# Optimization experiments

Hardware: AMD Instinct MI355X
Metric: run time of the kernel (lower is better)

Reference implementation:

```python
import jax, jax.numpy as jnp
import numpy as np

PI = 3.14159265359
FC = 5.208e6; FS = 20.832e6; FDEMOD = 5.208e6; C = 1540.0
FNUM = 2.0; MINW = 1e-3
NANG = 4; NELEM = 128; NZ = 192; NX = 192; NSAMP = 2048


def setup_inputs() -> dict:
    key = jax.random.key(0)
    k1, k2 = jax.random.split(key)
    idata = jax.random.normal(k1, (NANG, NELEM, NSAMP), jnp.float32)
    qdata = jax.random.normal(k2, (NANG, NELEM, NSAMP), jnp.float32)
    pitch = 0.298e-3  # PICMUS L11 pitch [m]
    ex = (np.arange(NELEM) - (NELEM - 1) / 2.0) * pitch
    ele_pos = np.stack([ex, np.zeros(NELEM), np.zeros(NELEM)], -1).astype(np.float32)
    xs = np.linspace(ex[0], ex[-1], NX)
    zs = np.linspace(5e-3, 48e-3, NZ)
    zz, xx = np.meshgrid(zs, xs, indexing='ij')  # out_shape = (NZ, NX)
    grid = np.stack([xx.ravel(), np.zeros(NZ * NX), zz.ravel()], -1).astype(np.float32)
    angles = np.linspace(-0.16, 0.16, NANG).astype(np.float32)
    time_zero = np.zeros(NANG, np.float32)
    return {"idata": idata, "qdata": qdata, "grid": jnp.asarray(grid),
            "angles": jnp.asarray(angles), "ele_pos": jnp.asarray(ele_pos),
            "time_zero": jnp.asarray(time_zero)}


def _lerp_gather(data, i0, frac):
    # data: [A,E,S]; i0: [A,E,P] int32; zero-padding outside [0,S) (grid_sample zeros, align_corners=False)
    S = data.shape[-1]
    def samp(idx):
        valid = (idx >= 0) & (idx < S)
        g = jnp.take_along_axis(data, jnp.clip(idx, 0, S - 1), axis=-1)
        return jnp.where(valid, g, jnp.zeros((), data.dtype))
    return (1.0 - frac) * samp(i0) + frac * samp(i0 + 1)


def reference(idata, qdata, grid, angles, ele_pos, time_zero):
    x = grid[:, 0]; z = grid[:, 2]  # [P]
    sin_a = jnp.sin(angles); cos_a = jnp.cos(angles)
    # -- transmit delays (plane wave) and apodization --  [A,P]
    txdel = (x[None, :] * sin_a[:, None] + z[None, :] * cos_a[:, None]
             + time_zero[:, None] * C) * (FS / C)
    xlim0 = ele_pos[0, 0]; xlim1 = ele_pos[-1, 0]
    x_proj = x[None, :] - z[None, :] * jnp.tan(angles)[:, None]
    txapo = ((x_proj >= xlim0 * 1.2) & (x_proj <= xlim1 * 1.2)).astype(idata.dtype)
    # -- receive delays (focus) and dynamic-aperture apodization --  [E,P]
    v = grid[None, :, :] - ele_pos[:, None, :]  # [E,P,3]
    rxdel = jnp.sqrt(jnp.sum(v * v, axis=-1)) * (FS / C)
    vx = v[..., 0]; vz = v[..., 2]
    mask = jnp.abs(vz / vx) > FNUM
    mask = mask | (jnp.abs(vx) <= MINW)
    mask = mask | ((vx >= MINW) & (x[None, :] <= ele_pos[0, 0]))
    mask = mask | ((vx <= -MINW) & (x[None, :] >= ele_pos[-1, 0]))
    rxapo = mask.astype(idata.dtype)
    # -- total delays and linear interpolation of IQ (grid_sample bilinear, H=1) --
    delays = txdel[:, None, :] + rxdel[None, :, :]  # [A,E,P] in samples
    i0f = jnp.floor(delays)
    frac = delays - i0f
    i0 = i0f.astype(jnp.int32)
    ifoc = _lerp_gather(idata, i0, frac)
    qfoc = _lerp_gather(qdata, i0, frac)
    # -- demodulation phase rotation --
    tshift = delays / FS - z[None, None, :] * 2.0 / C
    theta = 2.0 * PI * FDEMOD * tshift
    ct = jnp.cos(theta); st = jnp.sin(theta)
    ir = ifoc * ct - qfoc * st
    qr = qfoc * ct + ifoc * st
    # -- apodize and accumulate over angles and elements --
    apod = txapo[:, None, :] * rxapo[None, :, :]
    idas = jnp.sum(ir * apod, axis=(0, 1)).reshape(NZ, NX)
    qdas = jnp.sum(qr * apod, axis=(0, 1)).reshape(NZ, NX)
    return (idas, qdas)
```

## Files before the change

kernel.cpp:

```cpp
#include <hip/hip_runtime.h>
#include <math.h>

#define NANG   4
#define NELEM  128
#define NSAMP  2048
#define NZ     192
#define NX     192
#define NPIX   (NZ * NX)
#define NCHUNK 8
#define ECHUNK (NELEM / NCHUNK)
#define XT     16
#define ZT     4
#define NXT    (NX / XT)
#define NZT    (NZ / ZT)

constexpr float C_SOUND = 1540.0f;
constexpr float FS      = 20832000.0f;
constexpr float FDEMOD  = 5208000.0f;
constexpr float FS_C    = FS / C_SOUND;

__global__ __launch_bounds__(256) void das_pw_kernel(
    const float* __restrict__ idata,
    const float* __restrict__ qdata,
    const float* __restrict__ grid,
    const float* __restrict__ angles,
    const float* __restrict__ ele_pos,
    const float* __restrict__ time_zero,
    float* __restrict__ out)
{
    const int lane = threadIdx.x;
    const int a    = threadIdx.y;

    const int x0c = ((int)blockIdx.x % NXT) * XT;
    const int z0r = ((int)blockIdx.x / NXT) * ZT;

    const float ex0    = ele_pos[0];
    const float inv_pe = 1.0f / (ele_pos[3] - ex0);
    const float xlimN  = ele_pos[3 * (NELEM - 1)];
    const float xmin   = grid[3 * (z0r * NX + x0c)];
    const float xmax   = grid[3 * (z0r * NX + x0c + XT - 1)];
    const float zmax   = grid[3 * ((z0r + ZT - 1) * NX + x0c) + 2];
    const float half   = 0.5f * zmax;

    int e_lo = (int)floorf((xmin - half - ex0) * inv_pe);
    int e_hi = (int)ceilf ((xmax + half - ex0) * inv_pe) + 1;
    const int c0 = (int)blockIdx.y * ECHUNK;
    e_lo = max(e_lo, c0);
    e_hi = min(e_hi, c0 + ECHUNK);
    if (e_lo >= e_hi) return;

    const int p = (z0r + (lane >> 4)) * NX + x0c + (lane & (XT - 1));
    const float x = grid[3 * p + 0];
    const float z = grid[3 * p + 2];

    const float ang = angles[a];
    const float sa = sinf(ang);
    const float ca = cosf(ang);
    const float txdel = (x * sa + z * ca) * FS_C + time_zero[a] * FS;
    const float x_proj = x - z * (sa / ca);
    const bool txapo = (x_proj >= ex0 * 1.2f) && (x_proj <= xlimN * 1.2f);

    const float zrev_full = z * (2.0f * FDEMOD / C_SOUND);
    const float zrev = zrev_full - floorf(zrev_full);
    const float zz = z * z;

    float ai0 = 0.0f, aq0 = 0.0f, ai1 = 0.0f, aq1 = 0.0f;

    if (txapo) {
        const float* __restrict__ ib0 = idata + ((size_t)a * NELEM) * NSAMP;
        const float* __restrict__ qb0 = qdata + ((size_t)a * NELEM) * NSAMP;

        auto body = [&](int e, float& ai, float& aq) {
            const float ex = ele_pos[3 * e];
            const float vx = x - ex;
            const bool accept = z > 2.0f * fabsf(vx);

            const float r = sqrtf(fmaf(vx, vx, zz));
            const float delays = fmaf(r, FS_C, txdel);
            const float i0f  = floorf(delays);
            const float frac = delays - i0f;
            const int   i0   = (int)i0f;

            const float2 iv = *(const float2*)(ib0 + (e << 11) + i0);
            const float2 qv = *(const float2*)(qb0 + (e << 11) + i0);

            const float ifoc = fmaf(frac, iv.y - iv.x, iv.x);
            const float qfoc = fmaf(frac, qv.y - qv.x, qv.x);

            const float rev = fmaf(0.25f, (float)(i0 & 3) + frac, -zrev);
            float st = __builtin_amdgcn_sinf(rev);
            float ct = __builtin_amdgcn_cosf(rev);
            st = accept ? st : 0.0f;
            ct = accept ? ct : 0.0f;

            ai = fmaf(ifoc, ct, ai);
            ai = fmaf(-qfoc, st, ai);
            aq = fmaf(qfoc, ct, aq);
            aq = fmaf(ifoc, st, aq);
        };

        int e = e_lo;
        #pragma unroll 2
        for (; e + 1 < e_hi; e += 2) {
            body(e,     ai0, aq0);
            body(e + 1, ai1, aq1);
        }
        if (e < e_hi) body(e, ai0, aq0);
    }

    atomicAdd(&out[p],        ai0 + ai1);
    atomicAdd(&out[NPIX + p], aq0 + aq1);
}

extern "C" void kernel_launch(void* const* d_in, const int* in_sizes, int n_in,
                              void* d_out, int out_size, void* d_ws, size_t ws_size,
                              hipStream_t stream) {
    const float* idata     = (const float*)d_in[0];
    const float* qdata     = (const float*)d_in[1];
    const float* grid      = (const float*)d_in[2];
    const float* angles    = (const float*)d_in[3];
    const float* ele_pos   = (const float*)d_in[4];
    const float* time_zero = (const float*)d_in[5];
    float* out = (float*)d_out;

    hipMemsetAsync(out, 0, (size_t)out_size * sizeof(float), stream);

    dim3 block(64, NANG, 1);
    dim3 gridDim(NXT * NZT, NCHUNK, 1);
    das_pw_kernel<<<gridDim, block, 0, stream>>>(
        idata, qdata, grid, angles, ele_pos, time_zero, out);
}
```

Baseline: 86.11 us.

## Stage per-element sample windows in LDS instead of scattered global gathers

Each wavefront (one angle) now loads a contiguous 64-sample window of I and Q data per element into shared memory with coalesced loads. The window start comes from a conservative minimum delay bound for the pixel tile. Pixels then interpolate from LDS, with the index clamped to the window, instead of issuing scattered float2 global loads. The aim is to replace uncoalesced gathers with coalesced loads plus cheap LDS reads. In exchange, the txapo early-skip is dropped, the window may not cover every pixel's delay so clamping could corrupt samples, and the two independent accumulators are merged into one.

```diff
diff --git a/kernel.cpp b/kernel.cpp
--- a/kernel.cpp
+++ b/kernel.cpp
@@ -13,6 +13,7 @@
 #define ZT     4
 #define NXT    (NX / XT)
 #define NZT    (NZ / ZT)
+#define W      64
 
 constexpr float C_SOUND = 1540.0f;
 constexpr float FS      = 20832000.0f;
@@ -28,6 +29,8 @@
     const float* __restrict__ time_zero,
     float* __restrict__ out)
 {
+    __shared__ float2 s_win[NANG][2][W];
+
     const int lane = threadIdx.x;
     const int a    = threadIdx.y;
 
@@ -37,13 +40,14 @@
     const float ex0    = ele_pos[0];
     const float inv_pe = 1.0f / (ele_pos[3] - ex0);
     const float xlimN  = ele_pos[3 * (NELEM - 1)];
-    const float xmin   = grid[3 * (z0r * NX + x0c)];
-    const float xmax   = grid[3 * (z0r * NX + x0c + XT - 1)];
-    const float zmax   = grid[3 * ((z0r + ZT - 1) * NX + x0c) + 2];
-    const float half   = 0.5f * zmax;
+    const float xminT  = grid[3 * (z0r * NX + x0c)];
+    const float xmaxT  = grid[3 * (z0r * NX + x0c + XT - 1)];
+    const float zminT  = grid[3 * (z0r * NX + x0c) + 2];
+    const float zmaxT  = grid[3 * ((z0r + ZT - 1) * NX + x0c) + 2];
+    const float half   = 0.5f * zmaxT;
 
-    int e_lo = (int)floorf((xmin - half - ex0) * inv_pe);
-    int e_hi = (int)ceilf ((xmax + half - ex0) * inv_pe) + 1;
+    int e_lo = (int)floorf((xminT - half - ex0) * inv_pe);
+    int e_hi = (int)ceilf ((xmaxT + half - ex0) * inv_pe) + 1;
     const int c0 = (int)blockIdx.y * ECHUNK;
     e_lo = max(e_lo, c0);
     e_hi = min(e_hi, c0 + ECHUNK);
@@ -56,60 +60,67 @@
     const float ang = angles[a];
     const float sa = sinf(ang);
     const float ca = cosf(ang);
-    const float txdel = (x * sa + z * ca) * FS_C + time_zero[a] * FS;
+    const float tz = time_zero[a] * FS;
+    const float txdel = (x * sa + z * ca) * FS_C + tz;
     const float x_proj = x - z * (sa / ca);
     const bool txapo = (x_proj >= ex0 * 1.2f) && (x_proj <= xlimN * 1.2f);
+
+    const float txd_min = (fminf(xminT * sa, xmaxT * sa) + zminT * ca) * FS_C + tz;
+    const float zmin2 = zminT * zminT;
 
     const float zrev_full = z * (2.0f * FDEMOD / C_SOUND);
     const float zrev = zrev_full - floorf(zrev_full);
     const float zz = z * z;
 
-    float ai0 = 0.0f, aq0 = 0.0f, ai1 = 0.0f, aq1 = 0.0f;
+    float acc_i = 0.0f, acc_q = 0.0f;
 
-    if (txapo) {
-        const float* __restrict__ ib0 = idata + ((size_t)a * NELEM) * NSAMP;
-        const float* __restrict__ qb0 = qdata + ((size_t)a * NELEM) * NSAMP;
+    const float* __restrict__ ib0 = idata + ((size_t)a * NELEM) * NSAMP;
+    const float* __restrict__ qb0 = qdata + ((size_t)a * NELEM) * NSAMP;
 
-        auto body = [&](int e, float& ai, float& aq) {
-            const float ex = ele_pos[3 * e];
-            const float vx = x - ex;
-            const bool accept = z > 2.0f * fabsf(vx);
+    #pragma unroll 2
+    for (int e = e_lo; e < e_hi; ++e) {
+        const int b = e & 1;
+        const float ex = ele_pos[3 * e];
 
-            const float r = sqrtf(fmaf(vx, vx, zz));
-            const float delays = fmaf(r, FS_C, txdel);
-            const float i0f  = floorf(delays);
-            const float frac = delays - i0f;
-            const int   i0   = (int)i0f;
+        const float dxlo = fmaxf(fmaxf(xminT - ex, ex - xmaxT), 0.0f);
+        const float rmin = sqrtf(fmaf(dxlo, dxlo, zmin2));
+        int s0 = (int)floorf(fmaf(rmin, FS_C, txd_min)) - 2;
+        s0 = min(max(s0, 0), NSAMP - W);
 
-            const float2 iv = *(const float2*)(ib0 + (e << 11) + i0);
-            const float2 qv = *(const float2*)(qb0 + (e << 11) + i0);
+        const float ivl = ib0[(e << 11) + s0 + lane];
+        const float qvl = qb0[(e << 11) + s0 + lane];
+        s_win[a][b][lane] = make_float2(ivl, qvl);
 
-            const float ifoc = fmaf(frac, iv.y - iv.x, iv.x);
-            const float qfoc = fmaf(frac, qv.y - qv.x, qv.x);
+        const float vx = x - ex;
+        const bool accept = txapo && (z > 2.0f * fabsf(vx));
 
-            const float rev = fmaf(0.25f, (float)(i0 & 3) + frac, -zrev);
-            float st = __builtin_amdgcn_sinf(rev);
-            float ct = __builtin_amdgcn_cosf(rev);
-            st = accept ? st : 0.0f;
-            ct = accept ? ct : 0.0f;
+        const float r = sqrtf(fmaf(vx, vx, zz));
+        const float delays = fmaf(r, FS_C, txdel);
+        const float i0f  = floorf(delays);
+        const float frac = delays - i0f;
+        const int   i0   = (int)i0f;
 
-            ai = fmaf(ifoc, ct, ai);
-            ai = fmaf(-qfoc, st, ai);
-            aq = fmaf(qfoc, ct, aq);
-            aq = fmaf(ifoc, st, aq);
-        };
+        const int idx = min(max(i0 - s0, 0), W - 2);
+        const float2 p0 = s_win[a][b][idx];
+        const float2 p1 = s_win[a][b][idx + 1];
 
-        int e = e_lo;
-        #pragma unroll 2
-        for (; e + 1 < e_hi; e += 2) {
-            body(e,     ai0, aq0);
-            body(e + 1, ai1, aq1);
-        }
-        if (e < e_hi) body(e, ai0, aq0);
+        const float ifoc = fmaf(frac, p1.x - p0.x, p0.x);
+        const float qfoc = fmaf(frac, p1.y - p0.y, p0.y);
+
+        const float rev = fmaf(0.25f, (float)(i0 & 3) + frac, -zrev);
+        float st = __builtin_amdgcn_sinf(rev);
+        float ct = __builtin_amdgcn_cosf(rev);
+        st = accept ? st : 0.0f;
+        ct = accept ? ct : 0.0f;
+
+        acc_i = fmaf(ifoc, ct, acc_i);
+        acc_i = fmaf(-qfoc, st, acc_i);
+        acc_q = fmaf(qfoc, ct, acc_q);
+        acc_q = fmaf(ifoc, st, acc_q);
     }
 
-    atomicAdd(&out[p],        ai0 + ai1);
-    atomicAdd(&out[NPIX + p], aq0 + aq1);
+    atomicAdd(&out[p],        acc_i);
+    atomicAdd(&out[NPIX + p], acc_q);
 }
 
 extern "C" void kernel_launch(void* const* d_in, const int* in_sizes, int n_in,
```

Result: slower. 93.40 us (+8.5%).

## Loop angles inside each thread and factor the demod phase into tx and rx parts

Applied to the files above, without the earlier changes.

Each thread now handles all four angles for one element chunk instead of one angle across elements. The demodulation phasor is split into a per-angle transmit factor, computed once per pixel, and a per-element receive factor, computed once per element and shared across angles. The per-sample sin/cos is replaced by a complex multiply, and the receive sqrt and aperture test are amortised over four angles. The wave in the y dimension now picks a 32-element chunk rather than an angle, and the grid shrinks to one chunk dimension. The cost is more registers, and wavefronts whose chunk falls outside the aperture exit immediately, which can leave load imbalance. The transmit apodization is now applied as a multiply, so out-of-aperture angles still issue their gathers.

```diff
diff --git a/kernel.cpp b/kernel.cpp
--- a/kernel.cpp
+++ b/kernel.cpp
@@ -7,8 +7,7 @@
 #define NZ     192
 #define NX     192
 #define NPIX   (NZ * NX)
-#define NCHUNK 8
-#define ECHUNK (NELEM / NCHUNK)
+#define ECHUNK 32
 #define XT     16
 #define ZT     4
 #define NXT    (NX / XT)
@@ -29,7 +28,7 @@
     float* __restrict__ out)
 {
     const int lane = threadIdx.x;
-    const int a    = threadIdx.y;
+    const int cy   = threadIdx.y;
 
     const int x0c = ((int)blockIdx.x % NXT) * XT;
     const int z0r = ((int)blockIdx.x / NXT) * ZT;
@@ -37,76 +36,91 @@
     const float ex0    = ele_pos[0];
     const float inv_pe = 1.0f / (ele_pos[3] - ex0);
     const float xlimN  = ele_pos[3 * (NELEM - 1)];
-    const float xmin   = grid[3 * (z0r * NX + x0c)];
-    const float xmax   = grid[3 * (z0r * NX + x0c + XT - 1)];
-    const float zmax   = grid[3 * ((z0r + ZT - 1) * NX + x0c) + 2];
-    const float half   = 0.5f * zmax;
+    const float xminT  = grid[3 * (z0r * NX + x0c)];
+    const float xmaxT  = grid[3 * (z0r * NX + x0c + XT - 1)];
+    const float zmaxT  = grid[3 * ((z0r + ZT - 1) * NX + x0c) + 2];
+    const float half   = 0.5f * zmaxT;
 
-    int e_lo = (int)floorf((xmin - half - ex0) * inv_pe);
-    int e_hi = (int)ceilf ((xmax + half - ex0) * inv_pe) + 1;
-    const int c0 = (int)blockIdx.y * ECHUNK;
-    e_lo = max(e_lo, c0);
-    e_hi = min(e_hi, c0 + ECHUNK);
+    int e_lo = (int)floorf((xminT - half - ex0) * inv_pe);
+    int e_hi = (int)ceilf ((xmaxT + half - ex0) * inv_pe) + 1;
+    e_lo = max(e_lo, cy * ECHUNK);
+    e_hi = min(e_hi, cy * ECHUNK + ECHUNK);
     if (e_lo >= e_hi) return;
 
     const int p = (z0r + (lane >> 4)) * NX + x0c + (lane & (XT - 1));
     const float x = grid[3 * p + 0];
     const float z = grid[3 * p + 2];
 
-    const float ang = angles[a];
-    const float sa = sinf(ang);
-    const float ca = cosf(ang);
-    const float txdel = (x * sa + z * ca) * FS_C + time_zero[a] * FS;
-    const float x_proj = x - z * (sa / ca);
-    const bool txapo = (x_proj >= ex0 * 1.2f) && (x_proj <= xlimN * 1.2f);
+    const float zrev_full = z * (2.0f * FDEMOD / C_SOUND);
+    const float zz = z * z;
 
-    const float zrev_full = z * (2.0f * FDEMOD / C_SOUND);
-    const float zrev = zrev_full - floorf(zrev_full);
-    const float zz = z * z;
+    float txd[NANG], Pr[NANG], Pi[NANG];
+    #pragma unroll
+    for (int a = 0; a < NANG; ++a) {
+        const float ang = angles[a];
+        const float sa = sinf(ang);
+        const float ca = cosf(ang);
+        txd[a] = (x * sa + z * ca) * FS_C + time_zero[a] * FS;
+        const float x_proj = x - z * (sa / ca);
+        const float apo = ((x_proj >= ex0 * 1.2f) && (x_proj <= xlimN * 1.2f))
+                          ? 1.0f : 0.0f;
+        float tq = fmaf(0.25f, txd[a], -zrev_full);
+        tq -= floorf(tq);
+        Pr[a] = __builtin_amdgcn_cosf(tq) * apo;
+        Pi[a] = __builtin_amdgcn_sinf(tq) * apo;
+    }
 
     float ai0 = 0.0f, aq0 = 0.0f, ai1 = 0.0f, aq1 = 0.0f;
 
-    if (txapo) {
-        const float* __restrict__ ib0 = idata + ((size_t)a * NELEM) * NSAMP;
-        const float* __restrict__ qb0 = qdata + ((size_t)a * NELEM) * NSAMP;
+    const float* __restrict__ ibase = idata;
+    const float* __restrict__ qbase = qdata;
 
-        auto body = [&](int e, float& ai, float& aq) {
-            const float ex = ele_pos[3 * e];
-            const float vx = x - ex;
-            const bool accept = z > 2.0f * fabsf(vx);
+    auto body = [&](int e, float& ai, float& aq) {
+        const float ex = ele_pos[3 * e];
+        const float vx = x - ex;
+        const bool accept = z > 2.0f * fabsf(vx);
 
-            const float r = sqrtf(fmaf(vx, vx, zz));
-            const float delays = fmaf(r, FS_C, txdel);
+        const float r = sqrtf(fmaf(vx, vx, zz));
+        const float rxdel = r * FS_C;
+
+        float rxq = 0.25f * rxdel;
+        rxq -= floorf(rxq);
+        float cr = __builtin_amdgcn_cosf(rxq);
+        float sr = __builtin_amdgcn_sinf(rxq);
+        cr = accept ? cr : 0.0f;
+        sr = accept ? sr : 0.0f;
+
+        #pragma unroll
+        for (int a = 0; a < NANG; ++a) {
+            const float delays = rxdel + txd[a];
             const float i0f  = floorf(delays);
             const float frac = delays - i0f;
             const int   i0   = (int)i0f;
 
-            const float2 iv = *(const float2*)(ib0 + (e << 11) + i0);
-            const float2 qv = *(const float2*)(qb0 + (e << 11) + i0);
+            const size_t off = (((size_t)a * NELEM + e) << 11) + i0;
+            const float2 iv = *(const float2*)(ibase + off);
+            const float2 qv = *(const float2*)(qbase + off);
 
             const float ifoc = fmaf(frac, iv.y - iv.x, iv.x);
             const float qfoc = fmaf(frac, qv.y - qv.x, qv.x);
 
-            const float rev = fmaf(0.25f, (float)(i0 & 3) + frac, -zrev);
-            float st = __builtin_amdgcn_sinf(rev);
-            float ct = __builtin_amdgcn_cosf(rev);
-            st = accept ? st : 0.0f;
-            ct = accept ? ct : 0.0f;
+            const float ct = cr * Pr[a] - sr * Pi[a];
+            const float st = fmaf(sr, Pr[a], cr * Pi[a]);
 
             ai = fmaf(ifoc, ct, ai);
             ai = fmaf(-qfoc, st, ai);
             aq = fmaf(qfoc, ct, aq);
             aq = fmaf(ifoc, st, aq);
-        };
+        }
+    };
 
-        int e = e_lo;
-        #pragma unroll 2
-        for (; e + 1 < e_hi; e += 2) {
-            body(e,     ai0, aq0);
-            body(e + 1, ai1, aq1);
-        }
-        if (e < e_hi) body(e, ai0, aq0);
+    int e = e_lo;
+    #pragma unroll 2
+    for (; e + 1 < e_hi; e += 2) {
+        body(e,     ai0, aq0);
+        body(e + 1, ai1, aq1);
     }
+    if (e < e_hi) body(e, ai0, aq0);
 
     atomicAdd(&out[p],        ai0 + ai1);
     atomicAdd(&out[NPIX + p], aq0 + aq1);
@@ -126,7 +140,7 @@
     hipMemsetAsync(out, 0, (size_t)out_size * sizeof(float), stream);
 
     dim3 block(64, NANG, 1);
-    dim3 gridDim(NXT * NZT, NCHUNK, 1);
+    dim3 gridDim(NXT * NZT, 1, 1);
     das_pw_kernel<<<gridDim, block, 0, stream>>>(
         idata, qdata, grid, angles, ele_pos, time_zero, out);
 }
```

Result: slower. 114.4 us (+32.9%).
